# Kernel optimization log

Measured on AMD Instinct MI355X. Metric: run time of the kernel, lower is better.

Reference implementation:

```python
import jax, jax.numpy as jnp
import numpy as np

N, E, G = 100000, 1600000, 128
IN_DIM, H, C = 329, 4, 64
NEG_SLOPE = 0.2


def setup_inputs() -> dict:
    key = jax.random.key(0)
    ks = jax.random.split(key, 12)
    x = jax.random.normal(ks[0], (N, IN_DIM), dtype=jnp.float32)
    edge_index = jax.random.randint(ks[1], (2, E), 0, N, dtype=jnp.int64)
    batch = jnp.sort(jax.random.randint(ks[2], (N,), 0, G, dtype=jnp.int64))
    s = 1.0 / np.sqrt(IN_DIM)
    W = jax.random.uniform(ks[3], (IN_DIM, H * C), jnp.float32, -s, s)
    att_src = jax.random.normal(ks[4], (H, C), dtype=jnp.float32) * 0.1
    att_dst = jax.random.normal(ks[5], (H, C), dtype=jnp.float32) * 0.1
    bias = jnp.zeros((C,), jnp.float32)
    s1 = 1.0 / np.sqrt(C)
    w1 = jax.random.uniform(ks[6], (C, 64), jnp.float32, -s1, s1)
    b1 = jnp.zeros((64,), jnp.float32)
    s2 = 1.0 / np.sqrt(64)
    w2 = jax.random.uniform(ks[7], (64, 1), jnp.float32, -s2, s2)
    b2 = jnp.zeros((1,), jnp.float32)
    return {"x": x, "W": W, "att_src": att_src, "att_dst": att_dst,
            "bias": bias, "w1": w1, "b1": b1, "w2": w2, "b2": b2,
            "edge_index": edge_index, "batch": batch}


def reference(x, W, att_src, att_dst, bias, w1, b1, w2, b2, edge_index, batch):
    # --- GATConv (heads=4, concat=False, add_self_loops=True) ---
    xp = (x @ W).reshape(N, H, C)                       # [N,H,C]
    a_src = jnp.einsum('nhc,hc->nh', xp, att_src)       # [N,H]
    a_dst = jnp.einsum('nhc,hc->nh', xp, att_dst)       # [N,H]
    loops = jnp.arange(N, dtype=edge_index.dtype)
    src = jnp.concatenate([edge_index[0], loops])       # [E+N]
    dst = jnp.concatenate([edge_index[1], loops])
    logits = jax.nn.leaky_relu(a_src[src] + a_dst[dst], NEG_SLOPE)  # [E+N,H]
    # segment softmax over edges sharing a destination
    mx = jax.ops.segment_max(logits, dst, num_segments=N)
    ex = jnp.exp(logits - mx[dst])
    denom = jax.ops.segment_sum(ex, dst, num_segments=N)
    alpha = ex / denom[dst]                             # [E+N,H]
    msg = xp[src] * alpha[:, :, None]                   # [E+N,H,C]
    agg = jax.ops.segment_sum(msg, dst, num_segments=N) # [N,H,C]
    h = jax.nn.relu(agg.mean(axis=1) + bias)            # [N,C]
    # --- global mean pool over graphs ---
    counts = jax.ops.segment_sum(jnp.ones((N,), h.dtype), batch, num_segments=G)
    g = jax.ops.segment_sum(h, batch, num_segments=G) / jnp.maximum(counts, 1.0)[:, None]
    # --- head MLP ---
    y = jax.nn.sigmoid(jax.nn.relu(g @ w1 + b1) @ w2 + b2)  # [G,1]
    return y
```

## Files before the change

### kernel.cpp

```cpp
#include <hip/hip_runtime.h>
#include <math.h>

#define N_NODES 100000
#define N_EDGES 1600000
#define N_GRAPHS 128
#define IN_DIM 329
#define NH 4
#define CC 64
#define HC 256
#define NEG_SLOPE 0.2f
#define LOG2E 1.44269504f

#define K_PAD 384
#define M_PAD 100096
#define XBYTES (N_NODES * IN_DIM * 4)
#define NBUCK 196
#define BCAP 10240
#define EPB 8192

typedef unsigned short u16;
typedef unsigned char u8;
typedef unsigned int u32;
typedef __attribute__((ext_vector_type(8))) short short8;
typedef __attribute__((ext_vector_type(4))) float floatx4;
typedef __attribute__((ext_vector_type(2))) float floatx2;

__device__ __forceinline__ u16 f2bf(float f) {
    u32 u = __float_as_uint(f);
    u32 r = (u + 0x7FFFu + ((u >> 16) & 1u)) >> 16;
    return (u16)r;
}

__device__ __forceinline__ u32 pkbf(float a, float b) {
    return __builtin_amdgcn_perm(__float_as_uint(b), __float_as_uint(a), 0x07060302u);
}

__device__ __forceinline__ u8 f2fp8(float f) {
#if __has_builtin(__builtin_amdgcn_cvt_pk_fp8_f32)
    int pk = __builtin_amdgcn_cvt_pk_fp8_f32(f, f, 0, false);
    return (u8)(pk & 0xFF);
#else
    u32 u = __float_as_uint(f);
    u32 sgn = (u >> 24) & 0x80;
    float af = fabsf(f);
    if (af >= 448.f) return (u8)(sgn | 0x7E);
    if (af < 0.015625f) {
        int m = (int)rintf(af * 512.f);
        if (m >= 8) return (u8)(sgn | 0x08);
        return (u8)(sgn | (u32)m);
    }
    u32 au = u & 0x7FFFFFFF;
    u32 r = au + 0x0007FFFFu + ((au >> 20) & 1u);
    u32 e = r >> 23;
    u32 m3 = (r >> 20) & 7;
    int fe = (int)e - 127 + 7;
    if (fe >= 16) return (u8)(sgn | 0x7E);
    return (u8)(sgn | ((u32)fe << 3) | m3);
#endif
}

__device__ __forceinline__ float fp82f_sw(u32 b) {
    u32 s = (b & 0x80u) << 24;
    u32 e = (b >> 3) & 0xF;
    u32 m = b & 7;
    if (e == 0) {
        float v = (float)m * 0.001953125f;
        return (b & 0x80) ? -v : v;
    }
    return __uint_as_float(s | ((e + 120) << 23) | (m << 20));
}

__device__ __forceinline__ floatx4 dec4(int p) {
#if __has_builtin(__builtin_amdgcn_cvt_pk_f32_fp8)
    floatx2 lo = __builtin_amdgcn_cvt_pk_f32_fp8(p, false);
    floatx2 hi = __builtin_amdgcn_cvt_pk_f32_fp8(p, true);
    floatx4 r; r.x = lo.x; r.y = lo.y; r.z = hi.x; r.w = hi.y;
    return r;
#else
    floatx4 r;
    r.x = fp82f_sw(p & 0xFF);  r.y = fp82f_sw((p >> 8) & 0xFF);
    r.z = fp82f_sw((p >> 16) & 0xFF); r.w = fp82f_sw((p >> 24) & 0xFF);
    return r;
#endif
}

__device__ __forceinline__ void async_copy16(const void* g, void* l) {
    __builtin_amdgcn_global_load_lds((const __attribute__((address_space(1))) void*)g,
                                     (__attribute__((address_space(3))) void*)l, 16, 0, 0);
}

__device__ __forceinline__ float sel4(float4 a, int h) {
    float lo = (h & 1) ? a.y : a.x;
    float hi = (h & 1) ? a.w : a.z;
    return (h & 2) ? hi : lo;
}

__global__ __launch_bounds__(256) void convw_kernel(const float* __restrict__ W, u16* __restrict__ WbT)
{
    int i = blockIdx.x * 256 + threadIdx.x;
    if (i >= HC * 96) return;
    int c = i / 96;
    int k0 = (i - c * 96) * 4;
    ushort4 o = {0, 0, 0, 0};
    const float* wp = W + c;
    if (k0 < IN_DIM)     o.x = f2bf(wp[(size_t)k0 * HC]);
    if (k0 + 1 < IN_DIM) o.y = f2bf(wp[(size_t)(k0 + 1) * HC]);
    if (k0 + 2 < IN_DIM) o.z = f2bf(wp[(size_t)(k0 + 2) * HC]);
    if (k0 + 3 < IN_DIM) o.w = f2bf(wp[(size_t)(k0 + 3) * HC]);
    *(ushort4*)(WbT + (size_t)c * K_PAD + k0) = o;
}

__global__ __launch_bounds__(256) void gemm_mfma_kernel(
    const float* __restrict__ x, const u16* __restrict__ WbT, u8* __restrict__ xp8)
{
    __shared__ float Asf[128 * 64];
    __shared__ u16 Bs[128 * 64];

    const int tid = threadIdx.x;
    const int lane = tid & 63;
    const int wave = tid >> 6;
    const int lr = lane & 15;
    const int q = lane >> 4;
    const int row0 = blockIdx.x * 128;
    const int col0 = blockIdx.y * 128;
    const int rm0 = (wave & 1) * 64;
    const int cn0 = (wave >> 1) * 64;

    floatx4 acc[4][4];
#pragma unroll
    for (int i = 0; i < 4; i++)
#pragma unroll
        for (int j = 0; j < 4; j++) {
            acc[i][j].x = 0.f; acc[i][j].y = 0.f; acc[i][j].z = 0.f; acc[i][j].w = 0.f;
        }

    for (int k0 = 0; k0 < K_PAD; k0 += 64) {
#pragma unroll
        for (int t = 0; t < 8; t++) {
            int chunk = tid + t * 256;
            int row = chunk >> 4, ch = chunk & 15;
            int chl = ch ^ (row & 15);
            long gb = (long)(row0 + row) * (IN_DIM * 4) + (long)k0 * 4 + chl * 16;
            if (gb > (long)XBYTES - 16) gb = (long)XBYTES - 16;
            async_copy16((const char*)x + gb, (char*)Asf + (size_t)chunk * 16);
        }
#pragma unroll
        for (int t = 0; t < 4; t++) {
            int off = (tid + t * 256) * 16;
            int row = off >> 7;
            int col = off & 127;
            int gcol = col ^ ((row & 7) * 16);
            const char* gb = (const char*)WbT + (size_t)(col0 + row) * (K_PAD * 2) + k0 * 2 + gcol;
            async_copy16(gb, (char*)Bs + off);
        }
        __syncthreads();

        short8 af[2][4], bf[2][4];
#pragma unroll
        for (int ks = 0; ks < 2; ks++) {
#pragma unroll
            for (int i = 0; i < 4; i++) {
                int ra = rm0 + i * 16 + lr;
                int c0 = ks * 8 + q * 2;
                int sw = ra & 15;
                const float4* base = (const float4*)(Asf + ra * 64);
                float4 lo = base[c0 ^ sw];
                float4 hi = base[(c0 ^ sw) ^ 1];
                union { short8 v; u32 w[4]; } fr;
                fr.w[0] = pkbf(lo.x, lo.y);
                fr.w[1] = pkbf(lo.z, lo.w);
                fr.w[2] = pkbf(hi.x, hi.y);
                fr.w[3] = pkbf(hi.z, hi.w);
                af[ks][i] = fr.v;

                int rb = cn0 + i * 16 + lr;
                int cb = (ks * 64 + q * 16) ^ ((rb & 7) * 16);
                bf[ks][i] = *(const short8*)((const char*)Bs + rb * 128 + cb);
            }
        }
#pragma unroll
        for (int ks = 0; ks < 2; ks++)
#pragma unroll
            for (int i = 0; i < 4; i++)
#pragma unroll
                for (int j = 0; j < 4; j++)
                    acc[i][j] = __builtin_amdgcn_mfma_f32_16x16x32_bf16(af[ks][i], bf[ks][j], acc[i][j], 0, 0, 0);
        __syncthreads();
    }

#pragma unroll
    for (int i = 0; i < 4; i++) {
#pragma unroll
        for (int j = 0; j < 4; j++) {
            int col = col0 + cn0 + j * 16 + lr;
            float v[4] = {acc[i][j].x, acc[i][j].y, acc[i][j].z, acc[i][j].w};
#pragma unroll
            for (int r = 0; r < 4; r++) {
                int row = row0 + rm0 + i * 16 + q * 4 + r;
                if (row < N_NODES) xp8[(size_t)row * HC + col] = f2fp8(v[r]);
            }
        }
    }
}

__global__ __launch_bounds__(256) void a8_kernel(
    const u8* __restrict__ xp8, const float* __restrict__ att_src, const float* __restrict__ att_dst,
    float* __restrict__ a_src, float* __restrict__ a_dst)
{
    int n = blockIdx.x * 4 + (threadIdx.x >> 6);
    int lane = threadIdx.x & 63;
    if (n >= N_NODES) return;
    int h = lane >> 4;
    int c0 = (lane & 15) * 4;
    int p = *(const int*)(xp8 + (size_t)n * HC + h * CC + c0);
    floatx4 v = dec4(p);
    const float* as = att_src + h * CC + c0;
    const float* ad = att_dst + h * CC + c0;
    float ps = v.x * as[0] + v.y * as[1] + v.z * as[2] + v.w * as[3];
    float pd = v.x * ad[0] + v.y * ad[1] + v.z * ad[2] + v.w * ad[3];
#pragma unroll
    for (int m = 1; m < 16; m <<= 1) {
        ps += __shfl_xor(ps, m, 64);
        pd += __shfl_xor(pd, m, 64);
    }
    if ((lane & 15) == 0) {
        a_src[n * 4 + h] = ps * LOG2E;
        a_dst[n * 4 + h] = pd * LOG2E;
    }
}

__global__ __launch_bounds__(256) void bin2_kernel(
    const int* __restrict__ ei, int* __restrict__ bcur, int2* __restrict__ bins)
{
    __shared__ int hist[NBUCK];
    __shared__ int gpos[NBUCK];
    __shared__ int lcur[NBUCK];
    __shared__ int sc[256];

    const int t = threadIdx.x;
    const int lo = blockIdx.x * EPB;
    const int hi = min(lo + EPB, N_EDGES + N_NODES);

    for (int b = t; b < NBUCK; b += 256) hist[b] = 0;
    __syncthreads();

    for (int i = lo + t; i < hi; i += 256) {
        int d = (i < N_EDGES) ? ei[N_EDGES + i] : (i - N_EDGES);
        atomicAdd(&hist[d >> 9], 1);
    }
    __syncthreads();

    int v = (t < NBUCK) ? hist[t] : 0;
    if (t < NBUCK) { gpos[t] = atomicAdd(&bcur[t], v); lcur[t] = 0; }
    (void)sc;
    __syncthreads();

    for (int i = lo + t; i < hi; i += 256) {
        int s, d;
        if (i < N_EDGES) { s = ei[i]; d = ei[N_EDGES + i]; }
        else             { s = i - N_EDGES; d = s; }
        int b = d >> 9;
        int pos = gpos[b] + atomicAdd(&lcur[b], 1);
        if (pos < BCAP) {
            int2 r; r.x = s; r.y = d;
            bins[(size_t)b * BCAP + pos] = r;
        }
    }
}

__global__ __launch_bounds__(512) void fill3_kernel(
    const int* __restrict__ bcur, const int2* __restrict__ bins,
    int2* __restrict__ rs_deg, int* __restrict__ csr)
{
    __shared__ int deg[512];
    __shared__ int cur[512];
    __shared__ int sc[256];
    __shared__ int order[BCAP];

    const int t = threadIdx.x;
    const int b = blockIdx.x;
    const int cnt = min(bcur[b], BCAP);
    const int2* bp = bins + (size_t)b * BCAP;
    const int gbase = b * BCAP;

    deg[t] = 0;
    __syncthreads();
    for (int i = t; i < cnt; i += 512) atomicAdd(&deg[bp[i].y & 511], 1);
    __syncthreads();

    int d0 = 0, d1 = 0;
    if (t < 256) {
        d0 = deg[2 * t]; d1 = deg[2 * t + 1];
        sc[t] = d0 + d1;
    }
    __syncthreads();
    for (int off = 1; off < 256; off <<= 1) {
        int u = (t < 256 && t >= off) ? sc[t - off] : 0;
        __syncthreads();
        if (t < 256) sc[t] += u;
        __syncthreads();
    }
    if (t < 256) {
        int excl = sc[t] - (d0 + d1);
        cur[2 * t] = excl;
        cur[2 * t + 1] = excl + d0;
        int n0 = b * 512 + 2 * t;
        if (n0 < N_NODES)     { int2 rd; rd.x = gbase + excl;      rd.y = d0; rs_deg[n0] = rd; }
        if (n0 + 1 < N_NODES) { int2 rd; rd.x = gbase + excl + d0; rd.y = d1; rs_deg[n0 + 1] = rd; }
    }
    __syncthreads();

    for (int i = t; i < cnt; i += 512) {
        int2 r = bp[i];
        int pos = atomicAdd(&cur[r.y & 511], 1);
        order[pos] = r.x;
    }
    __syncthreads();

    for (int i = t; i < cnt; i += 512) csr[gbase + i] = order[i];
}

__global__ __launch_bounds__(256) void aggregate_kernel(
    const u8* __restrict__ xp8, const float* __restrict__ a_src, const float* __restrict__ a_dst,
    const int2* __restrict__ rs_deg, const int* __restrict__ csr,
    const float* __restrict__ bias, float* __restrict__ hbuf)
{
    int n = blockIdx.x * 4 + (threadIdx.x >> 6);
    int lane = threadIdx.x & 63;
    if (n >= N_NODES) return;
    int2 rd = rs_deg[n];
    int rstart = __builtin_amdgcn_readfirstlane(rd.x);
    int deg    = __builtin_amdgcn_readfirstlane(rd.y);
    const int* ep = csr + rstart;
    int h = lane >> 4;
    int xoff = lane * 4;

    float ad = a_dst[n * 4 + h];

    float acc0 = 0.f, acc1 = 0.f, acc2 = 0.f, acc3 = 0.f, den = 0.f;
    int e = 0;
    for (; e + 4 <= deg; e += 4) {
        int s0 = ep[e], s1 = ep[e + 1], s2 = ep[e + 2], s3 = ep[e + 3];
        float4 A0 = *(const float4*)(a_src + s0 * 4);
        float4 A1 = *(const float4*)(a_src + s1 * 4);
        float4 A2 = *(const float4*)(a_src + s2 * 4);
        float4 A3 = *(const float4*)(a_src + s3 * 4);
        int p0 = *(const int*)(xp8 + s0 * HC + xoff);
        int p1 = *(const int*)(xp8 + s1 * HC + xoff);
        int p2 = *(const int*)(xp8 + s2 * HC + xoff);
        int p3 = *(const int*)(xp8 + s3 * HC + xoff);
        float z0 = sel4(A0, h) + ad, z1 = sel4(A1, h) + ad;
        float z2 = sel4(A2, h) + ad, z3 = sel4(A3, h) + ad;
        float w0 = exp2f(fmaxf(z0, NEG_SLOPE * z0));
        float w1 = exp2f(fmaxf(z1, NEG_SLOPE * z1));
        float w2 = exp2f(fmaxf(z2, NEG_SLOPE * z2));
        float w3 = exp2f(fmaxf(z3, NEG_SLOPE * z3));
        den += (w0 + w1) + (w2 + w3);
        floatx4 v0 = dec4(p0), v1 = dec4(p1), v2 = dec4(p2), v3 = dec4(p3);
        acc0 = fmaf(w0, v0.x, acc0); acc1 = fmaf(w0, v0.y, acc1);
        acc2 = fmaf(w0, v0.z, acc2); acc3 = fmaf(w0, v0.w, acc3);
        acc0 = fmaf(w1, v1.x, acc0); acc1 = fmaf(w1, v1.y, acc1);
        acc2 = fmaf(w1, v1.z, acc2); acc3 = fmaf(w1, v1.w, acc3);
        acc0 = fmaf(w2, v2.x, acc0); acc1 = fmaf(w2, v2.y, acc1);
        acc2 = fmaf(w2, v2.z, acc2); acc3 = fmaf(w2, v2.w, acc3);
        acc0 = fmaf(w3, v3.x, acc0); acc1 = fmaf(w3, v3.y, acc1);
        acc2 = fmaf(w3, v3.z, acc2); acc3 = fmaf(w3, v3.w, acc3);
    }
    for (; e < deg; e++) {
        int s0 = ep[e];
        float4 A0 = *(const float4*)(a_src + s0 * 4);
        int p0 = *(const int*)(xp8 + s0 * HC + xoff);
        float z0 = sel4(A0, h) + ad;
        float w0 = exp2f(fmaxf(z0, NEG_SLOPE * z0));
        den += w0;
        floatx4 v0 = dec4(p0);
        acc0 = fmaf(w0, v0.x, acc0); acc1 = fmaf(w0, v0.y, acc1);
        acc2 = fmaf(w0, v0.z, acc2); acc3 = fmaf(w0, v0.w, acc3);
    }

    float r = 1.f / den;
    acc0 *= r; acc1 *= r; acc2 *= r; acc3 *= r;
#pragma unroll
    for (int m = 16; m <= 32; m <<= 1) {
        acc0 += __shfl_xor(acc0, m, 64);
        acc1 += __shfl_xor(acc1, m, 64);
        acc2 += __shfl_xor(acc2, m, 64);
        acc3 += __shfl_xor(acc3, m, 64);
    }
    if (lane < 16) {
        const float* bp = bias + lane * 4;
        float4 o;
        o.x = fmaxf(0.25f * acc0 + bp[0], 0.f);
        o.y = fmaxf(0.25f * acc1 + bp[1], 0.f);
        o.z = fmaxf(0.25f * acc2 + bp[2], 0.f);
        o.w = fmaxf(0.25f * acc3 + bp[3], 0.f);
        *(float4*)&hbuf[(size_t)n * CC + lane * 4] = o;
    }
}

__global__ __launch_bounds__(256) void pool1_kernel(
    const float* __restrict__ hbuf, const int* __restrict__ batch,
    float* __restrict__ gsum, int* __restrict__ gcnt)
{
    int w = threadIdx.x >> 6, lane = threadIdx.x & 63;
    int r0 = blockIdx.x * 128 + w * 32;
    if (r0 >= N_NODES) return;
    int r1 = min(r0 + 32, N_NODES);
    int cur = batch[r0];
    float s = 0.f;
    int c = 0;
    for (int r = r0; r < r1; r++) {
        int bb = batch[r];
        if (bb != cur) {
            atomicAdd(&gsum[cur * 64 + lane], s);
            if (lane == 0) atomicAdd(&gcnt[cur], c);
            s = 0.f; c = 0; cur = bb;
        }
        s += hbuf[(size_t)r * CC + lane];
        c++;
    }
    atomicAdd(&gsum[cur * 64 + lane], s);
    if (lane == 0) atomicAdd(&gcnt[cur], c);
}

__global__ __launch_bounds__(64) void pool2_kernel(
    const float* __restrict__ gsum, const int* __restrict__ gcnt,
    const float* __restrict__ w1, const float* __restrict__ b1,
    const float* __restrict__ w2, const float* __restrict__ b2,
    float* __restrict__ out)
{
    int g = blockIdx.x;
    int lane = threadIdx.x;
    __shared__ float gv[64];
    gv[lane] = gsum[g * 64 + lane] / (float)max(gcnt[g], 1);
    __syncthreads();
    float hid = b1[lane];
    for (int c = 0; c < 64; c++) hid = fmaf(gv[c], w1[c * 64 + lane], hid);
    hid = fmaxf(hid, 0.f);
    float part = hid * w2[lane];
#pragma unroll
    for (int off = 32; off > 0; off >>= 1) part += __shfl_xor(part, off, 64);
    if (lane == 0) out[g] = 1.f / (1.f + __expf(-(part + b2[0])));
}

extern "C" void kernel_launch(void* const* d_in, const int* in_sizes, int n_in,
                              void* d_out, int out_size, void* d_ws, size_t ws_size,
                              hipStream_t stream)
{
    const float* x       = (const float*)d_in[0];
    const float* W       = (const float*)d_in[1];
    const float* att_src = (const float*)d_in[2];
    const float* att_dst = (const float*)d_in[3];
    const float* bias    = (const float*)d_in[4];
    const float* w1      = (const float*)d_in[5];
    const float* b1      = (const float*)d_in[6];
    const float* w2      = (const float*)d_in[7];
    const float* b2      = (const float*)d_in[8];
    const int*   ei      = (const int*)d_in[9];
    const int*   batch   = (const int*)d_in[10];
    float* out = (float*)d_out;

    char* ws = (char*)d_ws;
    size_t off = 0;
    auto alloc = [&](size_t bytes) -> void* {
        void* p = ws + off;
        off += (bytes + 255) & ~(size_t)255;
        return p;
    };
    u16*   WbT       = (u16*)alloc((size_t)HC * K_PAD * 2);
    u8*    xp8       = (u8*)alloc((size_t)N_NODES * HC);
    float* a_src_b   = (float*)alloc((size_t)N_NODES * NH * 4);
    float* a_dst_b   = (float*)alloc((size_t)N_NODES * NH * 4);
    size_t zoff0 = off;
    int*   bcur      = (int*)alloc((size_t)NBUCK * 4);
    float* gsum      = (float*)alloc((size_t)N_GRAPHS * 64 * 4);
    int*   gcnt      = (int*)alloc((size_t)N_GRAPHS * 4);
    size_t zbytes = off - zoff0;
    int2*  bins      = (int2*)alloc((size_t)NBUCK * BCAP * 8);
    int2*  rs_deg    = (int2*)alloc((size_t)N_NODES * 8);
    int*   csr       = (int*)alloc((size_t)NBUCK * BCAP * 4);
    float* hbuf      = (float*)alloc((size_t)N_NODES * CC * 4);

    hipMemsetAsync(bcur, 0, zbytes, stream);

    convw_kernel<<<(HC * 96 + 255) / 256, 256, 0, stream>>>(W, WbT);

    dim3 ggrid(M_PAD / 128, 2);
    gemm_mfma_kernel<<<ggrid, 256, 0, stream>>>(x, WbT, xp8);

    a8_kernel<<<(N_NODES + 3) / 4, 256, 0, stream>>>(xp8, att_src, att_dst, a_src_b, a_dst_b);

    int tot = N_EDGES + N_NODES;
    bin2_kernel<<<(tot + EPB - 1) / EPB, 256, 0, stream>>>(ei, bcur, bins);
    fill3_kernel<<<NBUCK, 512, 0, stream>>>(bcur, bins, rs_deg, csr);

    aggregate_kernel<<<(N_NODES + 3) / 4, 256, 0, stream>>>(xp8, a_src_b, a_dst_b,
                                                            rs_deg, csr, bias, hbuf);

    pool1_kernel<<<(N_NODES + 127) / 128, 256, 0, stream>>>(hbuf, batch, gsum, gcnt);
    pool2_kernel<<<N_GRAPHS, 64, 0, stream>>>(gsum, gcnt, w1, b1, w2, b2, out);
}
```

Baseline: 427.1 us.

## Software-pipeline edge gathers in GAT aggregation with double-buffered index and data loads

Measured after the change: 409.9 us. -4.0%, faster.

```diff
diff --git a/kernel.cpp b/kernel.cpp
--- a/kernel.cpp
+++ b/kernel.cpp
@@ -89,12 +89,6 @@
                                      (__attribute__((address_space(3))) void*)l, 16, 0, 0);
 }
 
-__device__ __forceinline__ float sel4(float4 a, int h) {
-    float lo = (h & 1) ? a.y : a.x;
-    float hi = (h & 1) ? a.w : a.z;
-    return (h & 2) ? hi : lo;
-}
-
 __global__ __launch_bounds__(256) void convw_kernel(const float* __restrict__ W, u16* __restrict__ WbT)
 {
     int i = blockIdx.x * 256 + threadIdx.x;
@@ -337,46 +331,67 @@
 
     float ad = a_dst[n * 4 + h];
 
+    const int dm1 = deg - 1;
+    const int nb  = (deg + 3) >> 2;
+
     float acc0 = 0.f, acc1 = 0.f, acc2 = 0.f, acc3 = 0.f, den = 0.f;
-    int e = 0;
-    for (; e + 4 <= deg; e += 4) {
-        int s0 = ep[e], s1 = ep[e + 1], s2 = ep[e + 2], s3 = ep[e + 3];
-        float4 A0 = *(const float4*)(a_src + s0 * 4);
-        float4 A1 = *(const float4*)(a_src + s1 * 4);
-        float4 A2 = *(const float4*)(a_src + s2 * 4);
-        float4 A3 = *(const float4*)(a_src + s3 * 4);
-        int p0 = *(const int*)(xp8 + s0 * HC + xoff);
-        int p1 = *(const int*)(xp8 + s1 * HC + xoff);
-        int p2 = *(const int*)(xp8 + s2 * HC + xoff);
-        int p3 = *(const int*)(xp8 + s3 * HC + xoff);
-        float z0 = sel4(A0, h) + ad, z1 = sel4(A1, h) + ad;
-        float z2 = sel4(A2, h) + ad, z3 = sel4(A3, h) + ad;
-        float w0 = exp2f(fmaxf(z0, NEG_SLOPE * z0));
-        float w1 = exp2f(fmaxf(z1, NEG_SLOPE * z1));
-        float w2 = exp2f(fmaxf(z2, NEG_SLOPE * z2));
-        float w3 = exp2f(fmaxf(z3, NEG_SLOPE * z3));
-        den += (w0 + w1) + (w2 + w3);
-        floatx4 v0 = dec4(p0), v1 = dec4(p1), v2 = dec4(p2), v3 = dec4(p3);
-        acc0 = fmaf(w0, v0.x, acc0); acc1 = fmaf(w0, v0.y, acc1);
-        acc2 = fmaf(w0, v0.z, acc2); acc3 = fmaf(w0, v0.w, acc3);
-        acc0 = fmaf(w1, v1.x, acc0); acc1 = fmaf(w1, v1.y, acc1);
-        acc2 = fmaf(w1, v1.z, acc2); acc3 = fmaf(w1, v1.w, acc3);
-        acc0 = fmaf(w2, v2.x, acc0); acc1 = fmaf(w2, v2.y, acc1);
-        acc2 = fmaf(w2, v2.z, acc2); acc3 = fmaf(w2, v2.w, acc3);
-        acc0 = fmaf(w3, v3.x, acc0); acc1 = fmaf(w3, v3.y, acc1);
-        acc2 = fmaf(w3, v3.z, acc2); acc3 = fmaf(w3, v3.w, acc3);
-    }
-    for (; e < deg; e++) {
-        int s0 = ep[e];
-        float4 A0 = *(const float4*)(a_src + s0 * 4);
-        int p0 = *(const int*)(xp8 + s0 * HC + xoff);
-        float z0 = sel4(A0, h) + ad;
-        float w0 = exp2f(fmaxf(z0, NEG_SLOPE * z0));
-        den += w0;
-        floatx4 v0 = dec4(p0);
-        acc0 = fmaf(w0, v0.x, acc0); acc1 = fmaf(w0, v0.y, acc1);
-        acc2 = fmaf(w0, v0.z, acc2); acc3 = fmaf(w0, v0.w, acc3);
-    }
+
+    int iA0, iA1, iA2, iA3;
+    int iB0 = 0, iB1 = 0, iB2 = 0, iB3 = 0;
+    float aa0, aa1, aa2, aa3;  int pa0, pa1, pa2, pa3;
+    float ab0, ab1, ab2, ab3;  int pb0, pb1, pb2, pb3;
+
+#define AGG_LDI(eb_, j0, j1, j2, j3) do { \
+        j0 = ep[min((eb_), dm1)];     j1 = ep[min((eb_) + 1, dm1)]; \
+        j2 = ep[min((eb_) + 2, dm1)]; j3 = ep[min((eb_) + 3, dm1)]; } while (0)
+
+#define AGG_LDD(j0, j1, j2, j3, a0_, a1_, a2_, a3_, q0_, q1_, q2_, q3_) do { \
+        a0_ = a_src[(size_t)(j0) * 4 + h];  q0_ = *(const int*)(xp8 + (size_t)(j0) * HC + xoff); \
+        a1_ = a_src[(size_t)(j1) * 4 + h];  q1_ = *(const int*)(xp8 + (size_t)(j1) * HC + xoff); \
+        a2_ = a_src[(size_t)(j2) * 4 + h];  q2_ = *(const int*)(xp8 + (size_t)(j2) * HC + xoff); \
+        a3_ = a_src[(size_t)(j3) * 4 + h];  q3_ = *(const int*)(xp8 + (size_t)(j3) * HC + xoff); } while (0)
+
+#define AGG_CMP(eb_, a0_, a1_, a2_, a3_, q0_, q1_, q2_, q3_) do { \
+        float z0 = a0_ + ad, z1 = a1_ + ad, z2 = a2_ + ad, z3 = a3_ + ad; \
+        float w0 = exp2f(fmaxf(z0, NEG_SLOPE * z0)); \
+        float w1 = exp2f(fmaxf(z1, NEG_SLOPE * z1)); \
+        float w2 = exp2f(fmaxf(z2, NEG_SLOPE * z2)); \
+        float w3 = exp2f(fmaxf(z3, NEG_SLOPE * z3)); \
+        if ((eb_) + 3 >= deg) {                \
+            if ((eb_) + 1 >= deg) w1 = 0.f; \
+            if ((eb_) + 2 >= deg) w2 = 0.f; \
+            if ((eb_) + 3 >= deg) w3 = 0.f; \
+        } \
+        den += (w0 + w1) + (w2 + w3); \
+        floatx4 v0 = dec4(q0_), v1 = dec4(q1_), v2 = dec4(q2_), v3 = dec4(q3_); \
+        acc0 = fmaf(w0, v0.x, acc0); acc1 = fmaf(w0, v0.y, acc1); \
+        acc2 = fmaf(w0, v0.z, acc2); acc3 = fmaf(w0, v0.w, acc3); \
+        acc0 = fmaf(w1, v1.x, acc0); acc1 = fmaf(w1, v1.y, acc1); \
+        acc2 = fmaf(w1, v1.z, acc2); acc3 = fmaf(w1, v1.w, acc3); \
+        acc0 = fmaf(w2, v2.x, acc0); acc1 = fmaf(w2, v2.y, acc1); \
+        acc2 = fmaf(w2, v2.z, acc2); acc3 = fmaf(w2, v2.w, acc3); \
+        acc0 = fmaf(w3, v3.x, acc0); acc1 = fmaf(w3, v3.y, acc1); \
+        acc2 = fmaf(w3, v3.z, acc2); acc3 = fmaf(w3, v3.w, acc3); } while (0)
+
+    AGG_LDI(0, iA0, iA1, iA2, iA3);
+    AGG_LDD(iA0, iA1, iA2, iA3, aa0, aa1, aa2, aa3, pa0, pa1, pa2, pa3);
+    if (nb > 1) AGG_LDI(4, iB0, iB1, iB2, iB3);
+
+    for (int b = 0; b < nb; b += 2) {
+        int eb = b * 4;
+        if (b + 1 < nb) AGG_LDD(iB0, iB1, iB2, iB3, ab0, ab1, ab2, ab3, pb0, pb1, pb2, pb3);
+        if (b + 2 < nb) AGG_LDI(eb + 8, iA0, iA1, iA2, iA3);
+        AGG_CMP(eb, aa0, aa1, aa2, aa3, pa0, pa1, pa2, pa3);
+        if (b + 1 < nb) {
+            if (b + 2 < nb) AGG_LDD(iA0, iA1, iA2, iA3, aa0, aa1, aa2, aa3, pa0, pa1, pa2, pa3);
+            if (b + 3 < nb) AGG_LDI(eb + 12, iB0, iB1, iB2, iB3);
+            AGG_CMP(eb + 4, ab0, ab1, ab2, ab3, pb0, pb1, pb2, pb3);
+        }
+    }
+
+#undef AGG_LDI
+#undef AGG_LDD
+#undef AGG_CMP
 
     float r = 1.f / den;
     acc0 *= r; acc1 *= r; acc2 *= r; acc3 *= r;
```
